# Kernel tuning notes

Hardware: AMD Instinct MI355X
Metric: run time of the kernel (lower is better)

## Reference

```python
import jax, jax.numpy as jnp
import numpy as np

B, S, D = 1, 2048, 2048
H, G, HD = 32, 8, 64        # n_heads, n_kv_groups, head_dim
GS = H // G                  # group_size
ROPE_BASE = 10000.0


def _rope_tables(seq_len, head_dim):
    inv_freq = 1.0 / (ROPE_BASE ** (jnp.arange(0, head_dim, 2, dtype=jnp.float32) / head_dim))
    angles = jnp.arange(seq_len, dtype=jnp.float32)[:, None] * inv_freq[None, :]  # [S, HD/2]
    angles = jnp.concatenate([angles, angles], axis=-1)                            # [S, HD]
    return jnp.cos(angles), jnp.sin(angles)


def setup_inputs() -> dict:
    key = jax.random.key(0)
    ks = jax.random.split(key, 5)
    x = jax.random.normal(ks[0], (B, S, D), dtype=jnp.float32)
    mask = jnp.triu(jnp.ones((S, S), dtype=bool), k=1)  # True = masked (causal)
    cos_vals, sin_vals = _rope_tables(S, HD)
    scale = 0.02
    Wq = jax.random.normal(ks[1], (H * HD, D), dtype=jnp.float32) * scale
    Wk = jax.random.normal(ks[2], (G * HD, D), dtype=jnp.float32) * scale
    Wv = jax.random.normal(ks[3], (G * HD, D), dtype=jnp.float32) * scale
    Wo = jax.random.normal(ks[4], (D, H * HD), dtype=jnp.float32) * scale
    return {"x": x, "mask": mask, "cos_vals": cos_vals, "sin_vals": sin_vals,
            "Wq": Wq, "Wk": Wk, "Wv": Wv, "Wo": Wo}


def _apply_rope(t, cos, sin):
    # t: [b, heads, S, HD]; cos/sin: [S, HD]
    half = t.shape[-1] // 2
    t1, t2 = t[..., :half], t[..., half:]
    rotated = jnp.concatenate([-t2, t1], axis=-1)
    return t * cos[None, None] + rotated * sin[None, None]


def reference(x, mask, cos_vals, sin_vals, Wq, Wk, Wv, Wo):
    b, s, _ = x.shape
    q = (x @ Wq.T).reshape(b, s, H, HD).transpose(0, 2, 1, 3)   # [b,H,S,HD]
    k = (x @ Wk.T).reshape(b, s, G, HD).transpose(0, 2, 1, 3)   # [b,G,S,HD]
    v = (x @ Wv.T).reshape(b, s, G, HD).transpose(0, 2, 1, 3)   # [b,G,S,HD]
    q = _apply_rope(q, cos_vals, sin_vals)
    k = _apply_rope(k, cos_vals, sin_vals)
    # Group-broadcast instead of repeat_interleave (same math)
    q = q.reshape(b, G, GS, s, HD)
    scores = jnp.einsum('bghqd,bgkd->bghqk', q, k)              # [b,G,GS,S,S]
    scores = jnp.where(mask[None, None, None], -jnp.inf, scores)
    weights = jax.nn.softmax(scores / np.sqrt(HD).astype(np.float32), axis=-1)
    out = jnp.einsum('bghqk,bgkd->bghqd', weights, v)           # [b,G,GS,S,HD]
    out = out.reshape(b, H, s, HD).transpose(0, 2, 1, 3).reshape(b, s, H * HD)
    return out @ Wo.T
```

## Files before the change

### kernel.cpp

```cpp
#include <hip/hip_runtime.h>
#include <cstddef>
#include <cstdint>

#define S 2048
#define Dm 2048
#define NH 32
#define NG 8
#define HD 64

typedef __attribute__((ext_vector_type(8))) short bf16x8;
typedef __attribute__((ext_vector_type(4))) short bf16x4;
typedef __attribute__((ext_vector_type(4))) float f32x4;

__device__ __forceinline__ float fast_exp2(float x) { return __builtin_amdgcn_exp2f(x); }

__device__ __forceinline__ unsigned short f2bf(float f) {
  unsigned int u = __builtin_bit_cast(unsigned int, f);
  u = (u + 0x7fffu + ((u >> 16) & 1u)) >> 16;
  return (unsigned short)u;
}
__device__ __forceinline__ unsigned int pk2bf(float lo, float hi) {
  unsigned int a = __builtin_bit_cast(unsigned int, lo) + 0x8000u;
  unsigned int b = __builtin_bit_cast(unsigned int, hi) + 0x8000u;
  return (a >> 16) | (b & 0xffff0000u);
}
__device__ __forceinline__ void gl_lds16(const unsigned short* g, unsigned short* l) {
  __builtin_amdgcn_global_load_lds(
      (const __attribute__((address_space(1))) unsigned int*)g,
      (__attribute__((address_space(3))) unsigned int*)l, 16, 0, 0);
}

__device__ __forceinline__ void lds_drain_barrier() {
  asm volatile("s_waitcnt lgkmcnt(0)" ::: "memory");
  asm volatile("s_barrier" ::: "memory");
}

#define QSC 0.1803368801111601f

__global__ __launch_bounds__(256) void cvt_all(const float* __restrict__ x,
                                               const float* __restrict__ Wq,
                                               const float* __restrict__ Wk,
                                               const float* __restrict__ Wv,
                                               const float* __restrict__ Wo,
                                               unsigned short* __restrict__ xb,
                                               unsigned short* __restrict__ Wcat,
                                               unsigned short* __restrict__ Wob) {
  int i = blockIdx.x * 256 + threadIdx.x;
  const float4* src;
  ushort4* dst;
  if (i < 1048576)      { src = (const float4*)x  + i;             dst = (ushort4*)xb + i; }
  else if (i < 2097152) { src = (const float4*)Wq + (i - 1048576); dst = (ushort4*)Wcat + (i - 1048576); }
  else if (i < 2359296) { src = (const float4*)Wk + (i - 2097152); dst = (ushort4*)Wcat + 1048576 + (i - 2097152); }
  else if (i < 2621440) { src = (const float4*)Wv + (i - 2359296); dst = (ushort4*)Wcat + 1310720 + (i - 2359296); }
  else                  { src = (const float4*)Wo + (i - 2621440); dst = (ushort4*)Wob + (i - 2621440); }
  float4 v = *src;
  ushort4 o;
  o.x = f2bf(v.x); o.y = f2bf(v.y); o.z = f2bf(v.z); o.w = f2bf(v.w);
  *dst = o;
}

template<int MI, int NJ>
__global__ __launch_bounds__(256) void gemm_bf16(const unsigned short* __restrict__ A,
                                                 const unsigned short* __restrict__ B,
                                                 float* __restrict__ Cf,
                                                 unsigned short* __restrict__ Cb,
                                                 unsigned short* __restrict__ VtOut,
                                                 const float* __restrict__ cosv,
                                                 const float* __restrict__ sinv,
                                                 int M, int N, int K) {
  constexpr int BM = MI * 32, BN = NJ * 32;
  __shared__ __align__(16) unsigned short As[2][BM * 64];
  __shared__ __align__(16) unsigned short Bs[2][BN * 64];
  const int tid = threadIdx.x;
  const int lane = tid & 63, wave = tid >> 6;
  const int row0 = blockIdx.y * BM, col0 = blockIdx.x * BN;
  const int wr = (wave >> 1) * (MI * 16), wc = (wave & 1) * (NJ * 16);
  const int fr = lane & 15, q4 = lane >> 4;

  f32x4 acc[MI][NJ];
#pragma unroll
  for (int i = 0; i < MI; i++)
#pragma unroll
    for (int j = 0; j < NJ; j++) acc[i][j] = (f32x4){0.f, 0.f, 0.f, 0.f};

  const int nk = K >> 6;

  auto stage = [&](int k0, int buf) {
#pragma unroll
    for (int c = 0; c < MI; c++) {
      int p = tid + c * 256;
      int r = p >> 3, sl = ((p & 7) ^ (r & 7)) * 8;
      gl_lds16(&A[(size_t)(row0 + r) * K + k0 + sl], &As[buf][p * 8]);
    }
#pragma unroll
    for (int b = 0; b < NJ; b++) {
      int p = tid + b * 256;
      int r = p >> 3, sl = ((p & 7) ^ (r & 7)) * 8;
      gl_lds16(&B[(size_t)(col0 + r) * K + k0 + sl], &Bs[buf][p * 8]);
    }
  };

  auto compute = [&](const unsigned short* Ab, const unsigned short* Bb) {
#pragma unroll
    for (int kk = 0; kk < 2; kk++) {
      bf16x8 af[MI], bfr[NJ];
#pragma unroll
      for (int i = 0; i < MI; i++) {
        int R = wr + i * 16 + fr;
        af[i] = *(const bf16x8*)&Ab[R * 64 + ((q4 + kk * 4) ^ (R & 7)) * 8];
      }
#pragma unroll
      for (int j = 0; j < NJ; j++) {
        int R = wc + j * 16 + fr;
        bfr[j] = *(const bf16x8*)&Bb[R * 64 + ((q4 + kk * 4) ^ (R & 7)) * 8];
      }
#pragma unroll
      for (int i = 0; i < MI; i++)
#pragma unroll
        for (int j = 0; j < NJ; j++)
          acc[i][j] = __builtin_amdgcn_mfma_f32_16x16x32_bf16(af[i], bfr[j], acc[i][j], 0, 0, 0);
    }
  };

  stage(0, 0);
  stage(64, 1);

  for (int t = 0; t < nk; ++t) {
    if (t + 1 < nk) {
      if constexpr (MI + NJ == 6)      asm volatile("s_waitcnt vmcnt(6)" ::: "memory");
      else if constexpr (MI + NJ == 4) asm volatile("s_waitcnt vmcnt(4)" ::: "memory");
      else                             asm volatile("s_waitcnt vmcnt(8)" ::: "memory");
    } else {
      asm volatile("s_waitcnt vmcnt(0)" ::: "memory");
    }
    asm volatile("s_barrier" ::: "memory");

    compute(As[t & 1], Bs[t & 1]);

    lds_drain_barrier();
    if (t + 2 < nk) stage((t + 2) << 6, t & 1);
  }

  const int cc = lane & 15, cr = (lane >> 4) * 4;

  if (cosv) {
#pragma unroll
    for (int i = 0; i < MI; i++) {
      int grb = row0 + wr + i * 16 + cr;
#pragma unroll
      for (int j = 0; j < 2; j++) {
        int gc = col0 + wc + j * 16 + cc;
        if (gc < 2560) {
          int d = j * 16 + cc;
          float qs = (gc < 2048) ? QSC : 1.0f;
#pragma unroll
          for (int r = 0; r < 4; r++) {
            float c = cosv[(grb + r) * 64 + d];
            float s = sinv[(grb + r) * 64 + d];
            float t1 = acc[i][j][r], t2 = acc[i][j + 2][r];
            acc[i][j][r]     = (t1 * c - t2 * s) * qs;
            acc[i][j + 2][r] = (t2 * c + t1 * s) * qs;
          }
        }
      }
    }
  }

#pragma unroll
  for (int i = 0; i < MI; i++)
#pragma unroll
    for (int j = 0; j < NJ; j++) {
      int gc = col0 + wc + j * 16 + cc;
#pragma unroll
      for (int r = 0; r < 4; r++) {
        int gr = row0 + wr + i * 16 + cr + r;
        if (cosv) {
          if (gc >= 2560) {
            int vc = (gr & ~31) | ((gr & 12) << 1) | ((gr & 16) >> 2) | (gr & 3);
            VtOut[(size_t)(gc - 2560) * 2048 + vc] = f2bf(acc[i][j][r]);
          } else {
            Cb[(size_t)gr * N + gc] = f2bf(acc[i][j][r]);
          }
        } else if (Cf)    Cf[(size_t)gr * N + gc] = acc[i][j][r];
        else              Cb[(size_t)gr * N + gc] = f2bf(acc[i][j][r]);
      }
    }
}

__global__ __launch_bounds__(256, 4) void flash_mfma(const unsigned short* __restrict__ QKV,
                                                     const unsigned short* __restrict__ Vt_g,
                                                     unsigned short* __restrict__ Ob) {
  __shared__ __align__(16) unsigned short Ks[2][64 * 64];
  __shared__ __align__(16) unsigned short Vs[2][64 * 64];

  const int tid = threadIdx.x;
  const int lane = tid & 63, wave = tid >> 6;
  const int m15 = lane & 15, q4 = lane >> 4;

  const int L = blockIdx.x;
  const int h = L & 31, g = h >> 2;
  const int u0 = L >> 5, a = u0 >> 4, b = u0 & 15;
  const int v = (a == 0) ? 31 - b : b;
  const int qb = v * 64;
  const int ntiles = v + 1;

  bf16x8 qf0, qf1;
  {
    const size_t qrow = (size_t)(qb + wave * 16 + m15) * 3072 + h * 64;
    qf0 = *(const bf16x8*)&QKV[qrow + q4 * 8];
    qf1 = *(const bf16x8*)&QKV[qrow + 32 + q4 * 8];
  }

  f32x4 accO[4];
  float l_lane = 0.f;
#pragma unroll
  for (int vt = 0; vt < 4; vt++) accO[vt] = (f32x4){0.f, 0.f, 0.f, 0.f};

  const int p0 = wave * 128 + lane, p1 = p0 + 64;
  const int sr0 = p0 >> 3, so0 = ((p0 & 7) ^ (sr0 & 7)) * 8;
  const int sr1 = p1 >> 3, so1 = ((p1 & 7) ^ (sr1 & 7)) * 8;

#pragma unroll
  for (int t = 0; t < 2; t++) {
    const int k0 = t * 64;
    gl_lds16(&QKV[(size_t)(k0 + sr0) * 3072 + 2048 + g * 64 + so0], &Ks[t][p0 * 8]);
    gl_lds16(&QKV[(size_t)(k0 + sr1) * 3072 + 2048 + g * 64 + so1], &Ks[t][p1 * 8]);
    gl_lds16(&Vt_g[(size_t)(g * 64 + sr0) * 2048 + k0 + so0], &Vs[t][p0 * 8]);
    gl_lds16(&Vt_g[(size_t)(g * 64 + sr1) * 2048 + k0 + so1], &Vs[t][p1 * 8]);
  }

  for (int t = 0; t < ntiles; t++) {
    if (t + 1 < ntiles) asm volatile("s_waitcnt vmcnt(4)" ::: "memory");
    else                asm volatile("s_waitcnt vmcnt(0)" ::: "memory");
    asm volatile("s_barrier" ::: "memory");

    const unsigned short* Kb = Ks[t & 1];
    const unsigned short* Vb = Vs[t & 1];

    f32x4 sc[4];
#pragma unroll
    for (int kt = 0; kt < 4; kt++) {
      const int krow = kt * 16 + m15;
      bf16x8 kf0 = *(const bf16x8*)&Kb[krow * 64 + (q4 ^ (krow & 7)) * 8];
      bf16x8 kf1 = *(const bf16x8*)&Kb[krow * 64 + ((q4 + 4) ^ (krow & 7)) * 8];
      f32x4 z = (f32x4){0.f, 0.f, 0.f, 0.f};
      z = __builtin_amdgcn_mfma_f32_16x16x32_bf16(kf0, qf0, z, 0, 0, 0);
      sc[kt] = __builtin_amdgcn_mfma_f32_16x16x32_bf16(kf1, qf1, z, 0, 0, 0);
    }

    if (t == v) {
      const int qo = wave * 16 + m15;
#pragma unroll
      for (int kt = 0; kt < 4; kt++)
#pragma unroll
        for (int r = 0; r < 4; r++)
          if (kt * 16 + q4 * 4 + r > qo) sc[kt][r] = -1e30f;
    }

    float rs = 0.f;
#pragma unroll
    for (int kt = 0; kt < 4; kt++)
#pragma unroll
      for (int r = 0; r < 4; r++) {
        float p = fast_exp2(sc[kt][r]);
        sc[kt][r] = p;
        rs += p;
      }
    l_lane += rs;

    int4 pa0, pa1;
    pa0.x = pk2bf(sc[0][0], sc[0][1]); pa0.y = pk2bf(sc[0][2], sc[0][3]);
    pa0.z = pk2bf(sc[1][0], sc[1][1]); pa0.w = pk2bf(sc[1][2], sc[1][3]);
    pa1.x = pk2bf(sc[2][0], sc[2][1]); pa1.y = pk2bf(sc[2][2], sc[2][3]);
    pa1.z = pk2bf(sc[3][0], sc[3][1]); pa1.w = pk2bf(sc[3][2], sc[3][3]);
    bf16x8 pA0 = __builtin_bit_cast(bf16x8, pa0);
    bf16x8 pA1 = __builtin_bit_cast(bf16x8, pa1);

#pragma unroll
    for (int vt = 0; vt < 4; vt++) {
      const int vrow = vt * 16 + m15;
      const int base = vrow * 64, sw = vrow & 7;
      bf16x8 vB0 = *(const bf16x8*)&Vb[base + (q4 ^ sw) * 8];
      bf16x8 vB1 = *(const bf16x8*)&Vb[base + ((q4 + 4) ^ sw) * 8];
      accO[vt] = __builtin_amdgcn_mfma_f32_16x16x32_bf16(pA0, vB0, accO[vt], 0, 0, 0);
      accO[vt] = __builtin_amdgcn_mfma_f32_16x16x32_bf16(pA1, vB1, accO[vt], 0, 0, 0);
    }

    lds_drain_barrier();
    if (t + 2 < ntiles) {
      const int k2 = (t + 2) * 64;
      unsigned short* Kn = (unsigned short*)Ks[t & 1];
      unsigned short* Vn = (unsigned short*)Vs[t & 1];
      gl_lds16(&QKV[(size_t)(k2 + sr0) * 3072 + 2048 + g * 64 + so0], &Kn[p0 * 8]);
      gl_lds16(&QKV[(size_t)(k2 + sr1) * 3072 + 2048 + g * 64 + so1], &Kn[p1 * 8]);
      gl_lds16(&Vt_g[(size_t)(g * 64 + sr0) * 2048 + k2 + so0], &Vn[p0 * 8]);
      gl_lds16(&Vt_g[(size_t)(g * 64 + sr1) * 2048 + k2 + so1], &Vn[p1 * 8]);
    }
  }

  float lsum = l_lane;
  lsum += __shfl_xor(lsum, 16);
  lsum += __shfl_xor(lsum, 32);
  float lr[4];
#pragma unroll
  for (int r = 0; r < 4; r++) lr[r] = 1.0f / __shfl(lsum, q4 * 20 + r);
#pragma unroll
  for (int vt = 0; vt < 4; vt++)
#pragma unroll
    for (int r = 0; r < 4; r++) {
      int row = qb + wave * 16 + q4 * 4 + r;
      Ob[(size_t)row * 2048 + h * 64 + vt * 16 + m15] = f2bf(accO[vt][r] * lr[r]);
    }
}

extern "C" void kernel_launch(void* const* d_in, const int* in_sizes, int n_in,
                              void* d_out, int out_size, void* d_ws, size_t ws_size,
                              hipStream_t stream) {
  const float* x    = (const float*)d_in[0];
  const float* cosv = (const float*)d_in[2];
  const float* sinv = (const float*)d_in[3];
  const float* Wq   = (const float*)d_in[4];
  const float* Wk   = (const float*)d_in[5];
  const float* Wv   = (const float*)d_in[6];
  const float* Wo   = (const float*)d_in[7];
  float* out = (float*)d_out;

  unsigned short* xb   = (unsigned short*)d_ws;
  unsigned short* Wcat = xb + (size_t)2048 * 2048;
  unsigned short* Wob  = Wcat + (size_t)3072 * 2048;
  unsigned short* QKV  = Wob + (size_t)2048 * 2048;
  unsigned short* Vt_g = QKV + (size_t)3072 * 2048;

  dim3 blk(256);
  cvt_all<<<14336, blk, 0, stream>>>(x, Wq, Wk, Wv, Wo, xb, Wcat, Wob);
  gemm_bf16<2, 4><<<dim3(24, 32), blk, 0, stream>>>(xb, Wcat, nullptr, QKV, Vt_g, cosv, sinv, 2048, 3072, 2048);
  flash_mfma<<<1024, blk, 0, stream>>>(QKV, Vt_g, xb);
  gemm_bf16<2, 2><<<dim3(32, 32), blk, 0, stream>>>(xb, Wob, out, nullptr, nullptr, nullptr, nullptr, 2048, 2048, 2048);
}
```

Baseline: 210.5 us.

## Split flash attention waves 2x2 over query and key halves with LDS reduction

The flash-attention kernel now assigns each of the four waves a 32-query by 32-key quadrant of the 64x64 tile instead of 16 queries by all 64 keys. Each K fragment is reused across two query fragments and each V fragment across two accumulators, which reduces LDS reads per MFMA. Partial outputs and row sums from the two key-half waves are combined through LDS at the end. The cost is more accumulator registers, an extra barrier and an LDS reduction epilogue, and only half the waves write the output.

```diff
diff --git a/kernel.cpp b/kernel.cpp
--- a/kernel.cpp
+++ b/kernel.cpp
@@ -196,6 +196,7 @@
   const int tid = threadIdx.x;
   const int lane = tid & 63, wave = tid >> 6;
   const int m15 = lane & 15, q4 = lane >> 4;
+  const int qh = wave & 1, kh = wave >> 1;
 
   const int L = blockIdx.x;
   const int h = L & 31, g = h >> 2;
@@ -204,17 +205,20 @@
   const int qb = v * 64;
   const int ntiles = v + 1;
 
-  bf16x8 qf0, qf1;
-  {
-    const size_t qrow = (size_t)(qb + wave * 16 + m15) * 3072 + h * 64;
-    qf0 = *(const bf16x8*)&QKV[qrow + q4 * 8];
-    qf1 = *(const bf16x8*)&QKV[qrow + 32 + q4 * 8];
-  }
-
-  f32x4 accO[4];
-  float l_lane = 0.f;
-#pragma unroll
-  for (int vt = 0; vt < 4; vt++) accO[vt] = (f32x4){0.f, 0.f, 0.f, 0.f};
+  bf16x8 qf[2][2];
+#pragma unroll
+  for (int f = 0; f < 2; f++) {
+    const size_t qrow = (size_t)(qb + qh * 32 + f * 16 + m15) * 3072 + h * 64;
+    qf[f][0] = *(const bf16x8*)&QKV[qrow + q4 * 8];
+    qf[f][1] = *(const bf16x8*)&QKV[qrow + 32 + q4 * 8];
+  }
+
+  f32x4 accO[2][4];
+  float l_lane[2] = {0.f, 0.f};
+#pragma unroll
+  for (int f = 0; f < 2; f++)
+#pragma unroll
+    for (int vt = 0; vt < 4; vt++) accO[f][vt] = (f32x4){0.f, 0.f, 0.f, 0.f};
 
   const int p0 = wave * 128 + lane, p1 = p0 + 64;
   const int sr0 = p0 >> 3, so0 = ((p0 & 7) ^ (sr0 & 7)) * 8;
@@ -237,53 +241,63 @@
     const unsigned short* Kb = Ks[t & 1];
     const unsigned short* Vb = Vs[t & 1];
 
-    f32x4 sc[4];
-#pragma unroll
-    for (int kt = 0; kt < 4; kt++) {
-      const int krow = kt * 16 + m15;
-      bf16x8 kf0 = *(const bf16x8*)&Kb[krow * 64 + (q4 ^ (krow & 7)) * 8];
-      bf16x8 kf1 = *(const bf16x8*)&Kb[krow * 64 + ((q4 + 4) ^ (krow & 7)) * 8];
-      f32x4 z = (f32x4){0.f, 0.f, 0.f, 0.f};
-      z = __builtin_amdgcn_mfma_f32_16x16x32_bf16(kf0, qf0, z, 0, 0, 0);
-      sc[kt] = __builtin_amdgcn_mfma_f32_16x16x32_bf16(kf1, qf1, z, 0, 0, 0);
-    }
+    bf16x8 kf0[2], kf1[2];
+#pragma unroll
+    for (int kt = 0; kt < 2; kt++) {
+      const int krow = kh * 32 + kt * 16 + m15;
+      kf0[kt] = *(const bf16x8*)&Kb[krow * 64 + ((q4 ^ (krow & 7)) * 8)];
+      kf1[kt] = *(const bf16x8*)&Kb[krow * 64 + (((q4 + 4) ^ (krow & 7)) * 8)];
+    }
+    f32x4 sc[2][2];
+#pragma unroll
+    for (int f = 0; f < 2; f++)
+#pragma unroll
+      for (int kt = 0; kt < 2; kt++) {
+        f32x4 z = (f32x4){0.f, 0.f, 0.f, 0.f};
+        z = __builtin_amdgcn_mfma_f32_16x16x32_bf16(kf0[kt], qf[f][0], z, 0, 0, 0);
+        sc[f][kt] = __builtin_amdgcn_mfma_f32_16x16x32_bf16(kf1[kt], qf[f][1], z, 0, 0, 0);
+      }
 
     if (t == v) {
-      const int qo = wave * 16 + m15;
-#pragma unroll
-      for (int kt = 0; kt < 4; kt++)
-#pragma unroll
-        for (int r = 0; r < 4; r++)
-          if (kt * 16 + q4 * 4 + r > qo) sc[kt][r] = -1e30f;
-    }
-
-    float rs = 0.f;
-#pragma unroll
-    for (int kt = 0; kt < 4; kt++)
-#pragma unroll
-      for (int r = 0; r < 4; r++) {
-        float p = fast_exp2(sc[kt][r]);
-        sc[kt][r] = p;
-        rs += p;
-      }
-    l_lane += rs;
-
-    int4 pa0, pa1;
-    pa0.x = pk2bf(sc[0][0], sc[0][1]); pa0.y = pk2bf(sc[0][2], sc[0][3]);
-    pa0.z = pk2bf(sc[1][0], sc[1][1]); pa0.w = pk2bf(sc[1][2], sc[1][3]);
-    pa1.x = pk2bf(sc[2][0], sc[2][1]); pa1.y = pk2bf(sc[2][2], sc[2][3]);
-    pa1.z = pk2bf(sc[3][0], sc[3][1]); pa1.w = pk2bf(sc[3][2], sc[3][3]);
-    bf16x8 pA0 = __builtin_bit_cast(bf16x8, pa0);
-    bf16x8 pA1 = __builtin_bit_cast(bf16x8, pa1);
+#pragma unroll
+      for (int f = 0; f < 2; f++) {
+        const int qo = qh * 32 + f * 16 + m15;
+#pragma unroll
+        for (int kt = 0; kt < 2; kt++)
+#pragma unroll
+          for (int r = 0; r < 4; r++)
+            if (kh * 32 + kt * 16 + q4 * 4 + r > qo) sc[f][kt][r] = -1e30f;
+      }
+    }
+
+    bf16x8 pA[2];
+#pragma unroll
+    for (int f = 0; f < 2; f++) {
+      float rs = 0.f;
+#pragma unroll
+      for (int kt = 0; kt < 2; kt++)
+#pragma unroll
+        for (int r = 0; r < 4; r++) {
+          float p = fast_exp2(sc[f][kt][r]);
+          sc[f][kt][r] = p;
+          rs += p;
+        }
+      l_lane[f] += rs;
+      int4 pa;
+      pa.x = pk2bf(sc[f][0][0], sc[f][0][1]);
+      pa.y = pk2bf(sc[f][0][2], sc[f][0][3]);
+      pa.z = pk2bf(sc[f][1][0], sc[f][1][1]);
+      pa.w = pk2bf(sc[f][1][2], sc[f][1][3]);
+      pA[f] = __builtin_bit_cast(bf16x8, pa);
+    }
 
 #pragma unroll
     for (int vt = 0; vt < 4; vt++) {
       const int vrow = vt * 16 + m15;
       const int base = vrow * 64, sw = vrow & 7;
-      bf16x8 vB0 = *(const bf16x8*)&Vb[base + (q4 ^ sw) * 8];
-      bf16x8 vB1 = *(const bf16x8*)&Vb[base + ((q4 + 4) ^ sw) * 8];
-      accO[vt] = __builtin_amdgcn_mfma_f32_16x16x32_bf16(pA0, vB0, accO[vt], 0, 0, 0);
-      accO[vt] = __builtin_amdgcn_mfma_f32_16x16x32_bf16(pA1, vB1, accO[vt], 0, 0, 0);
+      bf16x8 vB = *(const bf16x8*)&Vb[base + (((kh * 4 + q4) ^ sw) * 8)];
+      accO[0][vt] = __builtin_amdgcn_mfma_f32_16x16x32_bf16(pA[0], vB, accO[0][vt], 0, 0, 0);
+      accO[1][vt] = __builtin_amdgcn_mfma_f32_16x16x32_bf16(pA[1], vB, accO[1][vt], 0, 0, 0);
     }
 
     lds_drain_barrier();
@@ -298,19 +312,48 @@
     }
   }
 
-  float lsum = l_lane;
-  lsum += __shfl_xor(lsum, 16);
-  lsum += __shfl_xor(lsum, 32);
-  float lr[4];
-#pragma unroll
-  for (int r = 0; r < 4; r++) lr[r] = 1.0f / __shfl(lsum, q4 * 20 + r);
-#pragma unroll
-  for (int vt = 0; vt < 4; vt++)
-#pragma unroll
-    for (int r = 0; r < 4; r++) {
-      int row = qb + wave * 16 + q4 * 4 + r;
-      Ob[(size_t)row * 2048 + h * 64 + vt * 16 + m15] = f2bf(accO[vt][r] * lr[r]);
-    }
+  float* red  = (float*)Ks;
+  float* lred = (float*)Vs;
+
+  float lsum[2];
+#pragma unroll
+  for (int f = 0; f < 2; f++) {
+    float s = l_lane[f];
+    s += __shfl_xor(s, 16);
+    s += __shfl_xor(s, 32);
+    lsum[f] = s;
+  }
+
+  if (kh == 1) {
+#pragma unroll
+    for (int f = 0; f < 2; f++) {
+#pragma unroll
+      for (int vt = 0; vt < 4; vt++)
+#pragma unroll
+        for (int r = 0; r < 4; r++)
+          red[((f * 4 + vt) * 4 + r) * 128 + qh * 64 + lane] = accO[f][vt][r];
+      if (q4 == 0) lred[(qh * 2 + f) * 16 + m15] = lsum[f];
+    }
+  }
+  __syncthreads();
+
+  if (kh == 0) {
+#pragma unroll
+    for (int f = 0; f < 2; f++) {
+      float lt = lsum[f] + lred[(qh * 2 + f) * 16 + m15];
+      float lr[4];
+#pragma unroll
+      for (int r = 0; r < 4; r++) lr[r] = 1.0f / __shfl(lt, q4 * 20 + r);
+#pragma unroll
+      for (int vt = 0; vt < 4; vt++)
+#pragma unroll
+        for (int r = 0; r < 4; r++) {
+          float o = accO[f][vt][r] + red[((f * 4 + vt) * 4 + r) * 128 + qh * 64 + lane];
+          int row = qb + qh * 32 + f * 16 + q4 * 4 + r;
+          Ob[(size_t)row * 2048 + h * 64 + vt * 16 + m15] = f2bf(o * lr[r]);
+        }
+    }
+  }
 }
 
 extern "C" void kernel_launch(void* const* d_in, const int* in_sizes, int n_in,
```

After: 210.6 us, median of 2. Within noise of the previous version (+0.1%).
